# Optimization experiments

Hardware: AMD Instinct MI355X
Metric: run time of the kernel (lower is better)

## Reference

```python
import jax, jax.numpy as jnp
from jax import lax
import numpy as np

# Keras LSTM cell semantics: gate order [i, f, c(candidate), o];
# recurrent_activation = sigmoid, activation = act (relu for all layers except
# the final decoder LSTM which uses tanh). h = o * act(c).

def lstm_layer(x, W, U, b, act, return_sequences):
    # x: [B, T, I], W: [I, 4H], U: [H, 4H], b: [4H]
    B = x.shape[0]
    H = U.shape[0]
    xW = jnp.einsum('bti,ih->bth', x, W) + b  # precompute input projections
    def step(carry, xw_t):
        h, c = carry
        z = xw_t + h @ U                      # [B, 4H]
        i, f, g, o = jnp.split(z, 4, axis=-1)
        i = jax.nn.sigmoid(i)
        f = jax.nn.sigmoid(f)
        g = act(g)
        o = jax.nn.sigmoid(o)
        c = f * c + i * g
        h = o * act(c)
        return (h, c), h
    h0 = jnp.zeros((B, H), x.dtype)
    (hT, _), hs = lax.scan(step, (h0, h0), jnp.swapaxes(xW, 0, 1))
    if return_sequences:
        return jnp.swapaxes(hs, 0, 1)         # [B, T, H]
    return hT                                  # [B, H]

# layer dims: (in, hidden) for enc0, enc1, enc_latent, dec0, dec1, dec_out
LAYER_DIMS = [(256, 512), (512, 256), (256, 64), (64, 256), (256, 512), (512, 256)]

def setup_inputs() -> dict:
    key = jax.random.key(0)
    keys = jax.random.split(key, 1 + 3 * len(LAYER_DIMS))
    inp = {'x': jax.random.normal(keys[0], (64, 256, 256), dtype=jnp.float32)}
    for li, (din, dh) in enumerate(LAYER_DIMS):
        kw, ku, _ = keys[1 + 3 * li], keys[2 + 3 * li], keys[3 + 3 * li]
        sW = 1.0 / np.sqrt(din)
        sU = 1.0 / np.sqrt(dh)
        inp[f'W{li}'] = jax.random.normal(kw, (din, 4 * dh), dtype=jnp.float32) * sW
        inp[f'U{li}'] = jax.random.normal(ku, (dh, 4 * dh), dtype=jnp.float32) * sU
        inp[f'b{li}'] = jnp.zeros((4 * dh,), dtype=jnp.float32)
    return inp

def reference(x, W0, U0, b0, W1, U1, b1, W2, U2, b2, W3, U3, b3, W4, U4, b4, W5, U5, b5):
    relu = jax.nn.relu
    # encoder: relu LSTMs, all return_sequences=True
    h = lstm_layer(x, W0, U0, b0, relu, True)
    h = lstm_layer(h, W1, U1, b1, relu, True)
    h = lstm_layer(h, W2, U2, b2, relu, True)   # latent_dim=64
    # decoder: relu LSTMs then final tanh LSTM with return_sequences=False
    h = lstm_layer(h, W3, U3, b3, relu, True)
    h = lstm_layer(h, W4, U4, b4, relu, True)
    out = lstm_layer(h, W5, U5, b5, jnp.tanh, False)  # [B, input_size]
    return out
```

## Files before the change

### kernel.cpp

```cpp
#include <hip/hip_runtime.h>
#include <stdint.h>

#define AGENT __HIP_MEMORY_SCOPE_AGENT
typedef unsigned long long u64;

__global__ __launch_bounds__(256) void xpose_in(const float* __restrict__ x,
                                                float* __restrict__ xT) {
  const int t = blockIdx.x;
  const int b = threadIdx.x & 63;
  const int w = threadIdx.x >> 6;
  const float* xr = x + ((size_t)b * 256 + t) * 256;
  float* o = xT + (size_t)t * 256 * 64;
  for (int kq = w * 16; kq < w * 16 + 16; ++kq) {
    float4 v = *(const float4*)(xr + kq * 4);
    o[(size_t)(kq * 4 + 0) * 64 + b] = v.x;
    o[(size_t)(kq * 4 + 1) * 64 + b] = v.y;
    o[(size_t)(kq * 4 + 2) * 64 + b] = v.z;
    o[(size_t)(kq * 4 + 3) * 64 + b] = v.w;
  }
}

__global__ __launch_bounds__(256) void pack_wu(const float* __restrict__ W,
                                               const float* __restrict__ U,
                                               float* __restrict__ out,
                                               int DIN, int H) {
  __shared__ float tile[64][65];
  const int KT = DIN + H;
  const int KTq = KT >> 2;
  const int c0 = blockIdx.x * 64;
  const int k0 = blockIdx.y * 64;
  const int tx = threadIdx.x & 63;
  const int ty = threadIdx.x >> 6;
  for (int r = ty; r < 64; r += 4) {
    const int k = k0 + r;
    tile[r][tx] = (k < DIN) ? W[(size_t)k * (4 * H) + c0 + tx]
                            : U[(size_t)(k - DIN) * (4 * H) + c0 + tx];
  }
  __syncthreads();
  for (int r = ty; r < 64; r += 4) {
    const int cg = c0 + r;
    const int g = cg / H;
    const int col = cg - g * H;
    const int wg = col >> 2;
    const int jl = col & 3;
    const int c = (g << 2) | jl;
    const int k = k0 + tx;
    const int q = k >> 2;
    const int j = k & 3;
    out[(((size_t)wg * KTq + q) * 16 + c) * 4 + j] = tile[tx][r];
  }
}

#define SB __builtin_amdgcn_sched_barrier(0)
#define FMA_B8(I_, WS_, XA_, XB_)                                   \
  acc[(I_) * 8 + 0] = fmaf(WS_, (XA_).x, acc[(I_) * 8 + 0]);        \
  acc[(I_) * 8 + 1] = fmaf(WS_, (XA_).y, acc[(I_) * 8 + 1]);        \
  acc[(I_) * 8 + 2] = fmaf(WS_, (XA_).z, acc[(I_) * 8 + 2]);        \
  acc[(I_) * 8 + 3] = fmaf(WS_, (XA_).w, acc[(I_) * 8 + 3]);        \
  acc[(I_) * 8 + 4] = fmaf(WS_, (XB_).x, acc[(I_) * 8 + 4]);        \
  acc[(I_) * 8 + 5] = fmaf(WS_, (XB_).y, acc[(I_) * 8 + 5]);        \
  acc[(I_) * 8 + 6] = fmaf(WS_, (XB_).z, acc[(I_) * 8 + 6]);        \
  acc[(I_) * 8 + 7] = fmaf(WS_, (XB_).w, acc[(I_) * 8 + 7]);
#define FMA_ROW32(I_, WV_)                 \
  FMA_B8(I_, (WV_).x, x0a_, x0b_)          \
  FMA_B8(I_, (WV_).y, x1a_, x1b_)          \
  FMA_B8(I_, (WV_).z, x2a_, x2b_)          \
  FMA_B8(I_, (WV_).w, x3a_, x3b_)
#define QUAD_FMA(SPQ_, WPQ_)                                        \
  {                                                                 \
    const float4 x0a_ = (SPQ_)[0], x0b_ = (SPQ_)[1];                \
    const float4 x1a_ = (SPQ_)[16], x1b_ = (SPQ_)[17];              \
    const float4 x2a_ = (SPQ_)[32], x2b_ = (SPQ_)[33];              \
    const float4 x3a_ = (SPQ_)[48], x3b_ = (SPQ_)[49];              \
    const float4 w0_ = (WPQ_)[0], w1_ = (WPQ_)[1];                  \
    const float4 w2_ = (WPQ_)[2], w3_ = (WPQ_)[3];                  \
    const float4 w4_ = (WPQ_)[4], w5_ = (WPQ_)[5];                  \
    const float4 w6_ = (WPQ_)[6], w7_ = (WPQ_)[7];                  \
    FMA_ROW32(0, w0_)                                               \
    FMA_ROW32(1, w1_)                                               \
    FMA_ROW32(2, w2_)                                               \
    FMA_ROW32(3, w3_)                                               \
    FMA_ROW32(4, w4_)                                               \
    FMA_ROW32(5, w5_)                                               \
    FMA_ROW32(6, w6_)                                               \
    FMA_ROW32(7, w7_)                                               \
  }

template <int QL>
__device__ __forceinline__ void accum88(const float4* __restrict__ sp,
                                        const float4* __restrict__ wp,
                                        float acc[64]) {
  if constexpr (QL & 1) {
    QUAD_FMA(sp, wp)
    SB;
    sp += 64;
    wp += 17;
  }
#pragma unroll 1
  for (int p = 0; p < QL / 2; ++p) {
    QUAD_FMA(sp, wp)
    QUAD_FMA(sp + 64, wp + 17)
    SB;
    sp += 128;
    wp += 34;
  }
}

template <int NWG>
__device__ __forceinline__ void agg_body(unsigned* __restrict__ flg,
                                         unsigned* __restrict__ ep) {
  const int tid = threadIdx.x;
  if (tid >= 64) return;
  for (int t = 0; t < 256; ++t) {
    unsigned* base = flg + (size_t)t * NWG;
    if (NWG <= 64) {
      if (tid < NWG) {
        while (__hip_atomic_load(base + tid, __ATOMIC_RELAXED, AGENT) == 0u)
          __builtin_amdgcn_s_sleep(1);
      }
    } else {
      while (__hip_atomic_load(base + tid, __ATOMIC_RELAXED, AGENT) == 0u)
        __builtin_amdgcn_s_sleep(1);
      while (__hip_atomic_load(base + 64 + tid, __ATOMIC_RELAXED, AGENT) == 0u)
        __builtin_amdgcn_s_sleep(1);
    }
    asm volatile("s_waitcnt vmcnt(0)" ::: "memory");
    if (tid == 0)
      __hip_atomic_store(ep, (unsigned)(t + 1), __ATOMIC_RELAXED, AGENT);
  }
}

template <int DIN, int H, int NWG, bool FIN, bool XCOH>
__device__ __forceinline__ void layer_body(
    int wg, int tid, const float* __restrict__ xin, float* __restrict__ hseq,
    const float* __restrict__ wP, const float* __restrict__ bias,
    float* __restrict__ dout, unsigned* __restrict__ selfF,
    unsigned* __restrict__ selfE, unsigned* __restrict__ prevE,
    float* __restrict__ wL, float (*sZ)[16][64], float* sH) {
  constexpr int KT = DIN + H;
  constexpr int KTq = KT / 4;
  constexpr int XQ4 = DIN / 4;
  constexpr int QLX = DIN / 64;
  constexpr int QLH = H / 64;
  constexpr int SLABX = QLX * 17 + 2;
  constexpr int SLABH = QLH * 17 + 2;
  constexpr int T = 256;
  static_assert(DIN % 64 == 0 && H % 64 == 0, "16-way K-slicing");

  const int lane = tid & 63;
  const int wv = tid >> 6;
  const int cq = lane >> 5;
  const int k4 = (lane >> 3) & 3;
  const int bq = lane & 7;
  const int slice = wv * 4 + k4;

  {
    float4* wl = (float4*)wL;
    const float4* wp = (const float4*)wP + (size_t)wg * KTq * 16;
    for (int i = tid; i < KTq * 16; i += 256) {
      const int qg = i >> 4;
      const int c = i & 15;
      int lidx;
      if (qg < XQ4) {
        lidx = (qg / QLX) * SLABX + (qg % QLX) * 17 + c + (c >> 3);
      } else {
        const int qh = qg - XQ4;
        lidx = 16 * SLABX + (qh / QLH) * SLABH + (qh % QLH) * 17 + c + (c >> 3);
      }
      wl[lidx] = wp[i];
    }
  }
  const float4* wbx = (const float4*)wL + (size_t)slice * SLABX + cq * 9;
  const float4* wbh =
      (const float4*)wL + (size_t)16 * SLABX + (size_t)slice * SLABH + cq * 9;

  float bz[4];
#pragma unroll
  for (int g = 0; g < 4; ++g) bz[g] = bias[g * H + wg * 4 + wv];
  float cst = 0.f;
  __syncthreads();

  for (int t = 0; t < T; ++t) {
    float acc[64];
#pragma unroll
    for (int c = 0; c < 64; ++c) acc[c] = 0.f;

    if (!XCOH) {
      accum88<QLX>((const float4*)(xin + (size_t)t * DIN * 64) +
                       (size_t)slice * QLX * 64 + bq * 2,
                   wbx, acc);
    }
    if (t > 0 && tid == 0) {
      while (__hip_atomic_load(selfE, __ATOMIC_RELAXED, AGENT) < (unsigned)t)
        __builtin_amdgcn_s_sleep(2);
    }
    if (XCOH && tid == 64) {
      while (__hip_atomic_load(prevE, __ATOMIC_RELAXED, AGENT) <
             (unsigned)(t + 1))
        __builtin_amdgcn_s_sleep(2);
    }
    __syncthreads();
    asm volatile("" ::: "memory");

    if (XCOH) {
      accum88<QLX>((const float4*)(xin + (size_t)t * DIN * 64) +
                       (size_t)slice * QLX * 64 + bq * 2,
                   wbx, acc);
    }
    if (t > 0) {
      accum88<QLH>((const float4*)(hseq + (size_t)(t - 1) * H * 64) +
                       (size_t)slice * QLH * 64 + bq * 2,
                   wbh, acc);
    }

#pragma unroll
    for (int r = 0; r < 64; ++r) {
      const int v = __builtin_amdgcn_update_dpp(
          0, __float_as_int(acc[r]), 0x128, 0xF, 0xF, false);
      acc[r] += __int_as_float(v);
    }
#pragma unroll
    for (int r = 0; r < 64; ++r) {
      const int v = __builtin_amdgcn_ds_swizzle(__float_as_int(acc[r]),
                                                0x401F);
      acc[r] += __int_as_float(v);
    }

    if (k4 == 0) {
#pragma unroll
      for (int i = 0; i < 8; ++i) {
#pragma unroll
        for (int h = 0; h < 2; ++h) {
          *(float4*)&sZ[wv][cq * 8 + i][bq * 8 + h * 4] =
              make_float4(acc[i * 8 + h * 4 + 0], acc[i * 8 + h * 4 + 1],
                          acc[i * 8 + h * 4 + 2], acc[i * 8 + h * 4 + 3]);
        }
      }
    }
    __syncthreads();

    float z[4];
#pragma unroll
    for (int g = 0; g < 4; ++g) {
      z[g] = bz[g];
#pragma unroll
      for (int k = 0; k < 4; ++k) z[g] += sZ[k][g * 4 + wv][lane];
    }
    const float ig = 1.f / (1.f + __expf(-z[0]));
    const float fg = 1.f / (1.f + __expf(-z[1]));
    const float gg = FIN ? tanhf(z[2]) : fmaxf(z[2], 0.f);
    const float og = 1.f / (1.f + __expf(-z[3]));
    cst = fg * cst + ig * gg;
    const float ca = FIN ? tanhf(cst) : fmaxf(cst, 0.f);
    const float h = og * ca;
    sH[lane * 4 + wv] = h;
    if (FIN && t == T - 1) dout[(size_t)lane * H + wg * 4 + wv] = h;
    __syncthreads();

    if (wv == 0) {
      float* hw = hseq + (size_t)t * H * 64 + (size_t)(wg * 4) * 64 + lane;
#pragma unroll
      for (int jl = 0; jl < 4; ++jl) {
        __hip_atomic_store(hw + jl * 64, sH[lane * 4 + jl], __ATOMIC_RELAXED,
                           AGENT);
      }
      asm volatile("s_waitcnt vmcnt(0)" ::: "memory");
      if (tid == 0)
        __hip_atomic_store(&selfF[t * NWG + wg], 1u, __ATOMIC_RELAXED, AGENT);
    }
  }
}

__global__ __launch_bounds__(256, 2) void lstm_fused(
    const float* __restrict__ xT, float* __restrict__ h0,
    float* __restrict__ h1, float* __restrict__ h2, float* __restrict__ h3,
    float* __restrict__ h4, float* __restrict__ h5,
    const float* __restrict__ wuT0, const float* __restrict__ wuT1,
    const float* __restrict__ wuT2, const float* __restrict__ wuT3,
    const float* __restrict__ wuT4, const float* __restrict__ wuT5,
    const float* __restrict__ b0, const float* __restrict__ b1,
    const float* __restrict__ b2, const float* __restrict__ b3,
    const float* __restrict__ b4, const float* __restrict__ b5,
    float* __restrict__ dout, unsigned* __restrict__ f0,
    unsigned* __restrict__ f1, unsigned* __restrict__ f2,
    unsigned* __restrict__ f3, unsigned* __restrict__ f4,
    unsigned* __restrict__ f5, unsigned* __restrict__ eps) {
  __shared__ alignas(16) float wLDS[4 * 3328];
  __shared__ alignas(16) float sZ[4][16][64];
  __shared__ alignas(16) float sH[256];
  const int b = blockIdx.x;
  const int tid = threadIdx.x;
  if (b < 128) {
    layer_body<256, 512, 128, false, false>(b, tid, xT, h0, wuT0, b0, nullptr,
                                            f0, eps + 0, nullptr, wLDS, sZ, sH);
  } else if (b < 256) {
    layer_body<256, 512, 128, false, true>(b - 128, tid, h3, h4, wuT4, b4,
                                           nullptr, f4, eps + 4, eps + 3, wLDS,
                                           sZ, sH);
  } else if (b < 320) {
    layer_body<512, 256, 64, false, true>(b - 256, tid, h0, h1, wuT1, b1,
                                          nullptr, f1, eps + 1, eps + 0, wLDS,
                                          sZ, sH);
  } else if (b < 384) {
    layer_body<64, 256, 64, false, true>(b - 320, tid, h2, h3, wuT3, b3,
                                         nullptr, f3, eps + 3, eps + 2, wLDS,
                                         sZ, sH);
  } else if (b < 448) {
    layer_body<512, 256, 64, true, true>(b - 384, tid, h4, h5, wuT5, b5, dout,
                                         f5, eps + 5, eps + 4, wLDS, sZ, sH);
  } else if (b < 464) {
    layer_body<256, 64, 16, false, true>(b - 448, tid, h1, h2, wuT2, b2,
                                         nullptr, f2, eps + 2, eps + 1, wLDS,
                                         sZ, sH);
  } else {
    const int l = b - 464;
    if (l == 0) agg_body<128>(f0, eps + 0);
    else if (l == 1) agg_body<64>(f1, eps + 1);
    else if (l == 2) agg_body<16>(f2, eps + 2);
    else if (l == 3) agg_body<64>(f3, eps + 3);
    else if (l == 4) agg_body<128>(f4, eps + 4);
    else agg_body<64>(f5, eps + 5);
  }
}

extern "C" void kernel_launch(void* const* d_in, const int* in_sizes, int n_in,
                              void* d_out, int out_size, void* d_ws,
                              size_t ws_size, hipStream_t stream) {
  (void)in_sizes; (void)n_in; (void)out_size; (void)ws_size;
  const float* x = (const float*)d_in[0];
  const float* W[6];
  const float* U[6];
  const float* B[6];
  for (int l = 0; l < 6; ++l) {
    W[l] = (const float*)d_in[1 + 3 * l];
    U[l] = (const float*)d_in[2 + 3 * l];
    B[l] = (const float*)d_in[3 + 3 * l];
  }
  char* ws = (char*)d_ws;
  unsigned* f0 = (unsigned*)ws;
  unsigned* f1 = f0 + 128 * 256;
  unsigned* f2 = f1 + 64 * 256;
  unsigned* f3 = f2 + 16 * 256;
  unsigned* f4 = f3 + 64 * 256;
  unsigned* f5 = f4 + 128 * 256;
  unsigned* eps = f0 + 464 * 256;
  float* wuT0 = (float*)(ws + (1u << 20));
  float* wuT1 = wuT0 + (size_t)2048 * 768;
  float* wuT2 = wuT1 + (size_t)1024 * 768;
  float* wuT3 = wuT2 + (size_t)256 * 320;
  float* wuT4 = wuT3 + (size_t)1024 * 320;
  float* wuT5 = wuT4 + (size_t)2048 * 768;
  float* xT = (float*)(ws + (22u << 20));
  float* h0 = (float*)(ws + (38u << 20));
  float* h1 = (float*)(ws + (70u << 20));
  float* h2 = (float*)(ws + (86u << 20));
  float* h3 = (float*)(ws + (90u << 20));
  float* h4 = (float*)(ws + (106u << 20));
  float* h5 = (float*)(ws + (138u << 20));

  hipMemsetAsync(f0, 0, (464 * 256 + 8) * sizeof(unsigned), stream);
  xpose_in<<<256, 256, 0, stream>>>(x, xT);
  pack_wu<<<dim3(32, 12), 256, 0, stream>>>(W[0], U[0], wuT0, 256, 512);
  pack_wu<<<dim3(16, 12), 256, 0, stream>>>(W[1], U[1], wuT1, 512, 256);
  pack_wu<<<dim3(4, 5), 256, 0, stream>>>(W[2], U[2], wuT2, 256, 64);
  pack_wu<<<dim3(16, 5), 256, 0, stream>>>(W[3], U[3], wuT3, 64, 256);
  pack_wu<<<dim3(32, 12), 256, 0, stream>>>(W[4], U[4], wuT4, 256, 512);
  pack_wu<<<dim3(16, 12), 256, 0, stream>>>(W[5], U[5], wuT5, 512, 256);

  lstm_fused<<<470, 256, 0, stream>>>(xT, h0, h1, h2, h3, h4, h5, wuT0, wuT1,
                                      wuT2, wuT3, wuT4, wuT5, B[0], B[1], B[2],
                                      B[3], B[4], B[5], (float*)d_out, f0, f1,
                                      f2, f3, f4, f5, eps);
}
```

Measured before the change: 3.508 ms.

## Double workgroup size to split K reduction across 32 slices for wide layers

Workgroups grow from 256 to 512 threads. For layers whose input-plus-hidden width is 768, the K dimension is split into 32 slices instead of 16, so each wave does half as many FMA passes per step, and the upper four waves add their partial sums into shared memory through an extra barrier. Narrower layers leave the extra waves idle. LDS slab padding is changed to fit the new slicing. This targets the per-timestep latency of the serial recurrence, at the cost of another __syncthreads per step, idle waves in the narrow layers, and fewer registers per thread under the new launch bounds.

```diff
diff --git a/kernel.cpp b/kernel.cpp
--- a/kernel.cpp
+++ b/kernel.cpp
@@ -90,19 +90,12 @@
 __device__ __forceinline__ void accum88(const float4* __restrict__ sp,
                                         const float4* __restrict__ wp,
                                         float acc[64]) {
-  if constexpr (QL & 1) {
+#pragma unroll 1
+  for (int q = 0; q < QL; ++q) {
     QUAD_FMA(sp, wp)
     SB;
     sp += 64;
     wp += 17;
-  }
-#pragma unroll 1
-  for (int p = 0; p < QL / 2; ++p) {
-    QUAD_FMA(sp, wp)
-    QUAD_FMA(sp + 64, wp + 17)
-    SB;
-    sp += 128;
-    wp += 34;
   }
 }
 
@@ -137,27 +130,30 @@
     float* __restrict__ dout, unsigned* __restrict__ selfF,
     unsigned* __restrict__ selfE, unsigned* __restrict__ prevE,
     float* __restrict__ wL, float (*sZ)[16][64], float* sH) {
-  constexpr int KT = DIN + H;
-  constexpr int KTq = KT / 4;
+  constexpr bool WIDE = (DIN + H == 768);
+  constexpr int NSL = WIDE ? 32 : 16;
+  constexpr int KTq = (DIN + H) / 4;
   constexpr int XQ4 = DIN / 4;
-  constexpr int QLX = DIN / 64;
-  constexpr int QLH = H / 64;
-  constexpr int SLABX = QLX * 17 + 2;
-  constexpr int SLABH = QLH * 17 + 2;
+  constexpr int QLX = DIN / 4 / NSL;
+  constexpr int QLH = H / 4 / NSL;
+  constexpr int SLABX = QLX * 17 + ((14 - QLX) & 7);
+  constexpr int SLABH = QLH * 17 + ((14 - QLH) & 7);
   constexpr int T = 256;
-  static_assert(DIN % 64 == 0 && H % 64 == 0, "16-way K-slicing");
+  static_assert(QLX >= 1 && QLH >= 1, "slice granularity");
 
   const int lane = tid & 63;
   const int wv = tid >> 6;
+  const int jw = wv & 3;
   const int cq = lane >> 5;
   const int k4 = (lane >> 3) & 3;
   const int bq = lane & 7;
   const int slice = wv * 4 + k4;
+  const bool active = WIDE || (wv < 4);
 
   {
     float4* wl = (float4*)wL;
     const float4* wp = (const float4*)wP + (size_t)wg * KTq * 16;
-    for (int i = tid; i < KTq * 16; i += 256) {
+    for (int i = tid; i < KTq * 16; i += 512) {
       const int qg = i >> 4;
       const int c = i & 15;
       int lidx;
@@ -165,18 +161,18 @@
         lidx = (qg / QLX) * SLABX + (qg % QLX) * 17 + c + (c >> 3);
       } else {
         const int qh = qg - XQ4;
-        lidx = 16 * SLABX + (qh / QLH) * SLABH + (qh % QLH) * 17 + c + (c >> 3);
+        lidx = NSL * SLABX + (qh / QLH) * SLABH + (qh % QLH) * 17 + c + (c >> 3);
       }
       wl[lidx] = wp[i];
     }
   }
   const float4* wbx = (const float4*)wL + (size_t)slice * SLABX + cq * 9;
-  const float4* wbh =
-      (const float4*)wL + (size_t)16 * SLABX + (size_t)slice * SLABH + cq * 9;
+  const float4* wbh = (const float4*)wL + (size_t)NSL * SLABX +
+                      (size_t)slice * SLABH + cq * 9;
 
   float bz[4];
 #pragma unroll
-  for (int g = 0; g < 4; ++g) bz[g] = bias[g * H + wg * 4 + wv];
+  for (int g = 0; g < 4; ++g) bz[g] = bias[g * H + wg * 4 + jw];
   float cst = 0.f;
   __syncthreads();
 
@@ -185,7 +181,7 @@
 #pragma unroll
     for (int c = 0; c < 64; ++c) acc[c] = 0.f;
 
-    if (!XCOH) {
+    if (!XCOH && active) {
       accum88<QLX>((const float4*)(xin + (size_t)t * DIN * 64) +
                        (size_t)slice * QLX * 64 + bq * 2,
                    wbx, acc);
@@ -202,31 +198,33 @@
     __syncthreads();
     asm volatile("" ::: "memory");
 
-    if (XCOH) {
+    if (XCOH && active) {
       accum88<QLX>((const float4*)(xin + (size_t)t * DIN * 64) +
                        (size_t)slice * QLX * 64 + bq * 2,
                    wbx, acc);
     }
-    if (t > 0) {
+    if (t > 0 && active) {
       accum88<QLH>((const float4*)(hseq + (size_t)(t - 1) * H * 64) +
                        (size_t)slice * QLH * 64 + bq * 2,
                    wbh, acc);
     }
 
-#pragma unroll
-    for (int r = 0; r < 64; ++r) {
-      const int v = __builtin_amdgcn_update_dpp(
-          0, __float_as_int(acc[r]), 0x128, 0xF, 0xF, false);
-      acc[r] += __int_as_float(v);
-    }
-#pragma unroll
-    for (int r = 0; r < 64; ++r) {
-      const int v = __builtin_amdgcn_ds_swizzle(__float_as_int(acc[r]),
-                                                0x401F);
-      acc[r] += __int_as_float(v);
-    }
-
-    if (k4 == 0) {
+    if (active) {
+#pragma unroll
+      for (int r = 0; r < 64; ++r) {
+        const int v = __builtin_amdgcn_update_dpp(
+            0, __float_as_int(acc[r]), 0x128, 0xF, 0xF, false);
+        acc[r] += __int_as_float(v);
+      }
+#pragma unroll
+      for (int r = 0; r < 64; ++r) {
+        const int v = __builtin_amdgcn_ds_swizzle(__float_as_int(acc[r]),
+                                                  0x401F);
+        acc[r] += __int_as_float(v);
+      }
+    }
+
+    if (wv < 4 && k4 == 0) {
 #pragma unroll
       for (int i = 0; i < 8; ++i) {
 #pragma unroll
@@ -238,23 +236,42 @@
       }
     }
     __syncthreads();
-
-    float z[4];
-#pragma unroll
-    for (int g = 0; g < 4; ++g) {
-      z[g] = bz[g];
-#pragma unroll
-      for (int k = 0; k < 4; ++k) z[g] += sZ[k][g * 4 + wv][lane];
-    }
-    const float ig = 1.f / (1.f + __expf(-z[0]));
-    const float fg = 1.f / (1.f + __expf(-z[1]));
-    const float gg = FIN ? tanhf(z[2]) : fmaxf(z[2], 0.f);
-    const float og = 1.f / (1.f + __expf(-z[3]));
-    cst = fg * cst + ig * gg;
-    const float ca = FIN ? tanhf(cst) : fmaxf(cst, 0.f);
-    const float h = og * ca;
-    sH[lane * 4 + wv] = h;
-    if (FIN && t == T - 1) dout[(size_t)lane * H + wg * 4 + wv] = h;
+    if constexpr (WIDE) {
+      if (wv >= 4 && k4 == 0) {
+#pragma unroll
+        for (int i = 0; i < 8; ++i) {
+#pragma unroll
+          for (int h = 0; h < 2; ++h) {
+            float4 v = *(const float4*)&sZ[wv - 4][cq * 8 + i][bq * 8 + h * 4];
+            v.x += acc[i * 8 + h * 4 + 0];
+            v.y += acc[i * 8 + h * 4 + 1];
+            v.z += acc[i * 8 + h * 4 + 2];
+            v.w += acc[i * 8 + h * 4 + 3];
+            *(float4*)&sZ[wv - 4][cq * 8 + i][bq * 8 + h * 4] = v;
+          }
+        }
+      }
+      __syncthreads();
+    }
+
+    if (wv < 4) {
+      float z[4];
+#pragma unroll
+      for (int g = 0; g < 4; ++g) {
+        z[g] = bz[g];
+#pragma unroll
+        for (int k = 0; k < 4; ++k) z[g] += sZ[k][g * 4 + jw][lane];
+      }
+      const float ig = 1.f / (1.f + __expf(-z[0]));
+      const float fg = 1.f / (1.f + __expf(-z[1]));
+      const float gg = FIN ? tanhf(z[2]) : fmaxf(z[2], 0.f);
+      const float og = 1.f / (1.f + __expf(-z[3]));
+      cst = fg * cst + ig * gg;
+      const float ca = FIN ? tanhf(cst) : fmaxf(cst, 0.f);
+      const float h = og * ca;
+      sH[lane * 4 + jw] = h;
+      if (FIN && t == T - 1) dout[(size_t)lane * H + wg * 4 + jw] = h;
+    }
     __syncthreads();
 
     if (wv == 0) {
@@ -271,7 +288,7 @@
   }
 }
 
-__global__ __launch_bounds__(256, 2) void lstm_fused(
+__global__ __launch_bounds__(512, 4) void lstm_fused(
     const float* __restrict__ xT, float* __restrict__ h0,
     float* __restrict__ h1, float* __restrict__ h2, float* __restrict__ h3,
     float* __restrict__ h4, float* __restrict__ h5,
@@ -285,7 +302,7 @@
     unsigned* __restrict__ f1, unsigned* __restrict__ f2,
     unsigned* __restrict__ f3, unsigned* __restrict__ f4,
     unsigned* __restrict__ f5, unsigned* __restrict__ eps) {
-  __shared__ alignas(16) float wLDS[4 * 3328];
+  __shared__ alignas(16) float wLDS[4 * 3456];
   __shared__ alignas(16) float sZ[4][16][64];
   __shared__ alignas(16) float sH[256];
   const int b = blockIdx.x;
@@ -367,7 +384,7 @@
   pack_wu<<<dim3(32, 12), 256, 0, stream>>>(W[4], U[4], wuT4, 256, 512);
   pack_wu<<<dim3(16, 12), 256, 0, stream>>>(W[5], U[5], wuT5, 512, 256);
 
-  lstm_fused<<<470, 256, 0, stream>>>(xT, h0, h1, h2, h3, h4, h5, wuT0, wuT1,
+  lstm_fused<<<470, 512, 0, stream>>>(xT, h0, h1, h2, h3, h4, h5, wuT0, wuT1,
                                       wuT2, wuT3, wuT4, wuT5, B[0], B[1], B[2],
                                       B[3], B[4], B[5], (float*)d_out, f0, f1,
                                       f2, f3, f4, f5, eps);
```

New measurement: 4.693 ms. 1.34x slower.
